# Performance work log

Measured on AMD Instinct MI355X. Metric: run time of the kernel, lower is better.

The kernel has to match this reference:

```python
import jax, jax.numpy as jnp
import numpy as np
from jax import lax

B, NQ, C = 2, 1024, 2048
H, DH = 16, 128
G, CD = 4, 512          # off_grps, off_dim = C // G
LR, HR = 24, 72         # low-res grid side, high-res grid side
INTER = 64
K = LR * LR             # sampled K/V tokens (grid_size == lr_size)


def setup_inputs() -> dict:
    key = jax.random.key(0)
    ks = jax.random.split(key, 16)
    s = 0.02
    d = {}
    d['hidden_states'] = jax.random.normal(ks[0], (B, NQ, C), jnp.float32)
    d['image_hd'] = jax.random.normal(ks[1], (B, HR * HR, C), jnp.float32)
    d['wq'] = jax.random.normal(ks[2], (C, C), jnp.float32) * s
    d['wk'] = jax.random.normal(ks[3], (C, C), jnp.float32) * s
    d['wv'] = jax.random.normal(ks[4], (C, C), jnp.float32) * s
    d['wo'] = jax.random.normal(ks[5], (C, C), jnp.float32) * s
    d['conv_dw_w'] = jax.random.normal(ks[6], (CD, 1, 3, 3), jnp.float32) * s
    d['ln1_w'] = jnp.ones((CD,), jnp.float32)
    d['ln1_b'] = jnp.zeros((CD,), jnp.float32)
    d['conv_lr_proj_w'] = jax.random.normal(ks[7], (INTER, CD), jnp.float32) * s
    d['proj_int_w'] = jax.random.normal(ks[8], (INTER, CD), jnp.float32) * s
    d['proj_int_b'] = jnp.zeros((INTER,), jnp.float32)
    d['ln2_w'] = jnp.ones((INTER,), jnp.float32)
    d['ln2_b'] = jnp.zeros((INTER,), jnp.float32)
    d['conv_off_w'] = jax.random.normal(ks[9], (2, INTER), jnp.float32) * s
    d['k_hd_w'] = jax.random.normal(ks[10], (C, C), jnp.float32) * s
    d['k_hd_b'] = jnp.zeros((C,), jnp.float32)
    d['v_hd_w'] = jax.random.normal(ks[11], (C, C), jnp.float32) * s
    d['v_hd_b'] = jnp.zeros((C,), jnp.float32)
    return d


def _ln_channels(x, w, b, eps=1e-5):
    # LayerNorm2d: normalize over channel axis of [N, C, H, W]
    mu = jnp.mean(x, axis=1, keepdims=True)
    var = jnp.var(x, axis=1, keepdims=True)
    xn = (x - mu) * lax.rsqrt(var + eps)
    return xn * w[None, :, None, None] + b[None, :, None, None]


def _tokens_to_grid(x, S):
    # [B, S*S, C] -> [B*G, CD, S, S]  (group channels like einops '(b) (h w) (g c) -> (b g) c h w')
    return x.reshape(B, S, S, G, CD).transpose(0, 3, 4, 1, 2).reshape(B * G, CD, S, S)


def _bilinear_sample(img, grid):
    # img [N, C, Hh, Wh]; grid [N, K, 2] (x, y) normalized to [-1, 1], align_corners=True
    N, Cc, Hh, Wh = img.shape
    x = (grid[..., 0] + 1.0) * 0.5 * (Wh - 1)
    y = (grid[..., 1] + 1.0) * 0.5 * (Hh - 1)
    x0f, y0f = jnp.floor(x), jnp.floor(y)
    wx = (x - x0f)[:, None, :]
    wy = (y - y0f)[:, None, :]
    x0 = jnp.clip(x0f.astype(jnp.int32), 0, Wh - 1)
    x1 = jnp.clip(x0 + 1, 0, Wh - 1)
    y0 = jnp.clip(y0f.astype(jnp.int32), 0, Hh - 1)
    y1 = jnp.clip(y0 + 1, 0, Hh - 1)
    imgf = img.reshape(N, Cc, Hh * Wh)
    gather = jax.vmap(lambda im, ix: im[:, ix])  # ([C,HW],[K]) -> [C,K]
    v00 = gather(imgf, y0 * Wh + x0)
    v01 = gather(imgf, y0 * Wh + x1)
    v10 = gather(imgf, y1 * Wh + x0)
    v11 = gather(imgf, y1 * Wh + x1)
    return (v00 * (1 - wx) * (1 - wy) + v01 * wx * (1 - wy)
            + v10 * (1 - wx) * wy + v11 * wx * wy)  # [N, C, K]


def _ref_grid():
    # normalized reference points as in _grid_generate (centers / (S-1) * 2 - 1)
    yy = (jnp.linspace(0.5, LR - 0.5, LR) / (LR - 1.0)) * 2.0 - 1.0
    xx = (jnp.linspace(0.5, LR - 0.5, LR) / (LR - 1.0)) * 2.0 - 1.0
    gy, gx = jnp.meshgrid(yy, xx, indexing='ij')
    return jnp.stack([gx, gy], axis=-1).reshape(K, 2)  # (x, y)


def reference(hidden_states, image_hd, wq, wk, wv, wo, conv_dw_w, ln1_w, ln1_b,
              conv_lr_proj_w, proj_int_w, proj_int_b, ln2_w, ln2_b, conv_off_w,
              k_hd_w, k_hd_b, v_hd_w, v_hd_b):
    # ---- QKV on the full sequence ----
    q = hidden_states @ wq.T
    k_txt = hidden_states @ wk.T
    v_txt = hidden_states @ wv.T

    # ---- offset network on LR image tokens (first LR*LR tokens) ----
    lr = _tokens_to_grid(hidden_states[:, :K, :], LR)          # [B*G, CD, LR, LR]
    x = lax.conv_general_dilated(lr, conv_dw_w, (1, 1), 'SAME',
                                 feature_group_count=CD,
                                 dimension_numbers=('NCHW', 'OIHW', 'NCHW'))
    x = jax.nn.silu(x)
    x = _ln_channels(x, ln1_w, ln1_b)
    x = jnp.einsum('nchw,oc->nohw', x, conv_lr_proj_w)          # 1x1 conv -> [B*G, INTER, LR, LR]
    # intention gate from spatially pooled group features
    pooled = jnp.mean(lr, axis=(2, 3))                          # [B*G, CD]
    gate = jax.nn.sigmoid(pooled @ proj_int_w.T + proj_int_b)   # [B*G, INTER]
    x = x * gate[:, :, None, None]
    x = _ln_channels(x, ln2_w, ln2_b)
    off = jnp.einsum('nchw,oc->nohw', x, conv_off_w)            # [B*G, 2, LR, LR]
    off = off.transpose(0, 2, 3, 1).reshape(B * G, K, 2)        # (x, y)
    pos = jnp.tanh(_ref_grid()[None] + off)                     # sampling locs in [-1, 1]

    # ---- deformable gather from HD features ----
    hd = _tokens_to_grid(image_hd, HR)                          # [B*G, CD, HR, HR]
    samp = _bilinear_sample(hd, pos)                            # [B*G, CD, K]
    samp = samp.reshape(B, G, CD, K).transpose(0, 3, 1, 2).reshape(B, K, C)
    k_hd = samp @ k_hd_w.T + k_hd_b
    v_hd = samp @ v_hd_w.T + v_hd_b

    # ---- attention: causal over text tokens, HD tokens fully visible ----
    k_all = jnp.concatenate([k_txt, k_hd], axis=1)              # [B, NQ+K, C]
    v_all = jnp.concatenate([v_txt, v_hd], axis=1)
    qh = q.reshape(B, NQ, H, DH).transpose(0, 2, 1, 3)
    kh = k_all.reshape(B, NQ + K, H, DH).transpose(0, 2, 1, 3)
    vh = v_all.reshape(B, NQ + K, H, DH).transpose(0, 2, 1, 3)
    scores = jnp.einsum('bhqd,bhkd->bhqk', qh, kh) / jnp.sqrt(jnp.float32(DH))
    col = jnp.arange(NQ + K)
    row = jnp.arange(NQ)
    allow = (col[None, :] >= NQ) | (col[None, :] <= row[:, None])
    scores = jnp.where(allow[None, None], scores, jnp.float32(-1e9))
    attn = jax.nn.softmax(scores, axis=-1)
    out = jnp.einsum('bhqk,bhkd->bhqd', attn, vh)
    out = out.transpose(0, 2, 1, 3).reshape(B, NQ, C)
    return out @ wo.T
```

## Files before the change

### kernel.cpp

```cpp
#include <hip/hip_runtime.h>

typedef unsigned short u16;
typedef unsigned int u32;
typedef __attribute__((ext_vector_type(8))) short bf8;
typedef __attribute__((ext_vector_type(4))) float f4;
typedef __attribute__((ext_vector_type(4))) unsigned short us4;

constexpr int B = 2;
constexpr int NQ = 1024;
constexpr int C = 2048;
constexpr int DH = 128;
constexpr int G = 4;
constexpr int CD = 512;
constexpr int LR = 24;
constexpr int HR = 72;
constexpr int INTER = 64;
constexpr int K = LR * LR;
constexpr int NKV = NQ + K;

#define MFMA16(a, b, c) __builtin_amdgcn_mfma_f32_16x16x32_bf16(a, b, c, 0, 0, 0)
#define GLDS(g, l)                                                         \
  __builtin_amdgcn_global_load_lds(                                        \
      (const __attribute__((address_space(1))) void*)(g),                  \
      (__attribute__((address_space(3))) void*)(l), 16, 0, 0)

__device__ __forceinline__ u16 f2bf1(float f) {
  u32 u = __float_as_uint(f);
  u32 r = (u + 0x7fffu + ((u >> 16) & 1u)) >> 16;
  return (u16)r;
}

__global__ __launch_bounds__(256) void f2bf_k8(
    const float* __restrict__ s0, const float* __restrict__ s1,
    const float* __restrict__ s2, const float* __restrict__ s3,
    const float* __restrict__ s4, const float* __restrict__ s5,
    const float* __restrict__ s6, const float* __restrict__ plrw,
    u16* __restrict__ d0, u16* __restrict__ d1, u16* __restrict__ d2,
    u16* __restrict__ d3, u16* __restrict__ d4, u16* __restrict__ d5,
    u16* __restrict__ d6, float* __restrict__ wt) {
  __shared__ u16 L[64][68];
  const int y = blockIdx.y;
  const int t = threadIdx.x;
  if (y == 7) {
    if (blockIdx.x >= 128) return;
    const int idx = blockIdx.x * 256 + t;
    wt[idx] = plrw[(idx & 63) * 512 + (idx >> 6)];
    return;
  }
  const float* s;
  u16* d;
  switch (y) {
    case 0: s = s0; d = d0; break;
    case 1: s = s1; d = d1; break;
    case 2: s = s2; d = d2; break;
    case 3: s = s3; d = d3; break;
    case 4: s = s4; d = d4; break;
    case 5: s = s5; d = d5; break;
    default: s = s6; d = d6; break;
  }
  if (y < 5) {
    const int pc = blockIdx.x;
    const int mb = pc >> 5, kb = pc & 31;
    const int rin = t >> 2, c0 = (t & 3) * 16;
    const float* src = s + (size_t)(mb * 64 + rin) * 2048 + kb * 64 + c0;
#pragma unroll
    for (int j = 0; j < 16; j += 4) {
      float4 v = *(const float4*)(src + j);
      L[rin][c0 + j] = f2bf1(v.x);
      L[rin][c0 + j + 1] = f2bf1(v.y);
      L[rin][c0 + j + 2] = f2bf1(v.z);
      L[rin][c0 + j + 3] = f2bf1(v.w);
    }
    __syncthreads();
    u16* dst = d + (size_t)pc * 4096 + t * 16;
#pragma unroll
    for (int gg = 0; gg < 2; ++gg) {
      const int g = t * 2 + gg;
      const int rh = g & 15, ks2 = (g >> 4) & 3, kc = (g >> 6) & 1, fr = g >> 7;
      const int row = fr * 16 + rh, cc = kc * 32 + ks2 * 8;
      us4 o0, o1;
      o0.x = L[row][cc];     o0.y = L[row][cc + 1];
      o0.z = L[row][cc + 2]; o0.w = L[row][cc + 3];
      o1.x = L[row][cc + 4]; o1.y = L[row][cc + 5];
      o1.z = L[row][cc + 6]; o1.w = L[row][cc + 7];
      *(us4*)(dst + gg * 8) = o0;
      *(us4*)(dst + gg * 8 + 4) = o1;
    }
  } else {
    const size_t i0 = ((size_t)blockIdx.x * 256 + t) * 16;
#pragma unroll
    for (int j = 0; j < 16; j += 4) {
      float4 v = *(const float4*)(s + i0 + j);
      us4 o;
      o.x = f2bf1(v.x); o.y = f2bf1(v.y); o.z = f2bf1(v.z); o.w = f2bf1(v.w);
      *(us4*)(d + i0 + j) = o;
    }
  }
}

#define SB()                               \
  do {                                     \
    __builtin_amdgcn_sched_barrier(0);     \
    __builtin_amdgcn_s_barrier();          \
    __builtin_amdgcn_sched_barrier(0);     \
  } while (0)
#define WVM(n) asm volatile("s_waitcnt vmcnt(" #n ")" ::: "memory")

__global__ __launch_bounds__(512, 2) void gemm_fused(
    const u16* __restrict__ Ast, const u16* __restrict__ Wq,
    const u16* __restrict__ Wk, const u16* __restrict__ Wv,
    const u16* __restrict__ samp, const u16* __restrict__ khw,
    const u16* __restrict__ vhw, const float* __restrict__ khb,
    const float* __restrict__ vhb, u16* __restrict__ outq,
    u16* __restrict__ kg, u16* __restrict__ vg) {
  __shared__ u16 As[2][4][4096];
  __shared__ u16 Bs[2][4][4096];
  const int tid = threadIdx.x, lane = tid & 63, w = tid >> 6;
  const int ks = lane >> 4, r = lane & 15;
  const int bid = blockIdx.x;

  if (bid < 192) {
    const int wm = w >> 2, wn = w & 3;
    const int swz = (bid & 7) * 24 + (bid >> 3);
    const int mt = swz / 24, nt = swz % 24;
    const u16* Wst = (nt < 8) ? Wq : (nt < 16) ? Wk : Wv;
    const int nb0 = (nt & 7) * 4;
    const int mb0 = mt * 4;

#define ST_A03(bi, kt)                                                        \
  do {                                                                        \
    GLDS(Ast + ((size_t)(mb0 + 0) * 32 + (kt)) * 4096 + tid * 8,              \
         &As[bi][0][tid * 8]);                                                \
    GLDS(Ast + ((size_t)(mb0 + 2) * 32 + (kt)) * 4096 + tid * 8,              \
         &As[bi][2][tid * 8]);                                                \
  } while (0)
#define ST_A47(bi, kt)                                                        \
  do {                                                                        \
    GLDS(Ast + ((size_t)(mb0 + 1) * 32 + (kt)) * 4096 + tid * 8,              \
         &As[bi][1][tid * 8]);                                                \
    GLDS(Ast + ((size_t)(mb0 + 3) * 32 + (kt)) * 4096 + tid * 8,              \
         &As[bi][3][tid * 8]);                                                \
  } while (0)
#define ST_B01(bi, kt)                                                        \
  do {                                                                        \
    GLDS(Wst + ((size_t)(nb0 + 0) * 32 + (kt)) * 4096 + tid * 8,              \
         &Bs[bi][0][tid * 8]);                                                \
    GLDS(Wst + ((size_t)(nb0 + 1) * 32 + (kt)) * 4096 + tid * 8,              \
         &Bs[bi][1][tid * 8]);                                                \
  } while (0)
#define ST_B23(bi, kt)                                                        \
  do {                                                                        \
    GLDS(Wst + ((size_t)(nb0 + 2) * 32 + (kt)) * 4096 + tid * 8,              \
         &Bs[bi][2][tid * 8]);                                                \
    GLDS(Wst + ((size_t)(nb0 + 3) * 32 + (kt)) * 4096 + tid * 8,              \
         &Bs[bi][3][tid * 8]);                                                \
  } while (0)
#define RD_A(dst, bi, half, kc)                                               \
  _Pragma("unroll") for (int i2 = 0; i2 < 4; ++i2) dst[i2] =                  \
      *(const bf8*)(&As[bi][wm * 2 + (half)]                                  \
                       [((i2 * 2 + (kc)) * 4 + ks) * 128 + r * 8]);
#define RD_B(dst, bi, kc)                                                     \
  _Pragma("unroll") for (int j2 = 0; j2 < 4; ++j2) dst[j2] =                  \
      *(const bf8*)(&Bs[bi][wn][((j2 * 2 + (kc)) * 4 + ks) * 128 + r * 8]);
#define MM(ACC, AF, BF)                                                       \
  do {                                                                        \
    __builtin_amdgcn_s_setprio(1);                                            \
    _Pragma("unroll") for (int i3 = 0; i3 < 4; ++i3)                          \
        _Pragma("unroll") for (int j3 = 0; j3 < 4; ++j3) ACC[i3][j3] =        \
            MFMA16(AF[i3], BF[j3], ACC[i3][j3]);                              \
    __builtin_amdgcn_s_setprio(0);                                            \
  } while (0)

    f4 accA[4][4], accB[4][4];
#pragma unroll
    for (int i = 0; i < 4; ++i)
#pragma unroll
      for (int j = 0; j < 4; ++j) {
        accA[i][j] = f4{0.f, 0.f, 0.f, 0.f};
        accB[i][j] = f4{0.f, 0.f, 0.f, 0.f};
      }
    bf8 af[4], b0[4], b1[4];

    ST_A03(0, 0); ST_B01(0, 0); ST_B23(0, 0); ST_A47(0, 0);
    ST_A03(1, 1); ST_B01(1, 1);
    WVM(6);
    SB();

    for (int t = 0; t < 32; ++t) {
      const int buf = t & 1;
      RD_A(af, buf, 0, 0);
      RD_B(b0, buf, 0);
      if (t + 1 < 32) ST_B23(buf ^ 1, t + 1);
      SB();
      MM(accA, af, b0);
      SB();
      RD_A(af, buf, 0, 1);
      RD_B(b1, buf, 1);
      if (t + 1 < 32) ST_A47(buf ^ 1, t + 1);
      SB();
      MM(accA, af, b1);
      if (t + 1 < 32) { WVM(8); } else { WVM(0); }
      SB();
      RD_A(af, buf, 1, 0);
      if (t + 2 < 32) ST_A03(buf, t + 2);
      SB();
      MM(accB, af, b0);
      SB();
      RD_A(af, buf, 1, 1);
      if (t + 2 < 32) ST_B01(buf, t + 2);
      SB();
      MM(accB, af, b1);
      if (t + 2 < 32) { WVM(6); } else if (t + 1 < 32) { WVM(2); }
      SB();
    }

#define EPI(ACC, HALF)                                                        \
  _Pragma("unroll") for (int i = 0; i < 4; ++i)                               \
      _Pragma("unroll") for (int j = 0; j < 4; ++j)                           \
          _Pragma("unroll") for (int rr = 0; rr < 4; ++rr) {                  \
    const int m = mt * 256 + wm * 128 + (HALF)*64 + i * 16 + ks * 4 + rr;     \
    const int n = nt * 256 + wn * 64 + j * 16 + r;                            \
    const float v = ACC[i][j][rr];                                            \
    const int sel = n >> 11, nn = n & 2047, hh = nn >> 7, dd = nn & 127;      \
    const int bb = m >> 10, qq = m & 1023;                                    \
    const u16 bv = f2bf1(v);                                                  \
    if (sel == 0) {                                                           \
      outq[(size_t)m * 2048 + nn] = bv;                                       \
    } else if (sel == 1) {                                                    \
      kg[(((size_t)(bb * 16 + hh) * 50 + (qq >> 5)) * 16 + (dd >> 3)) * 256 + \
         (qq & 31) * 8 + (dd & 7)] = bv;                                      \
    } else {                                                                  \
      vg[((size_t)(bb * 16 + hh) * 200 + (qq >> 3)) * 1024 + dd * 8 +         \
         (qq & 7)] = bv;                                                      \
    }                                                                         \
  }
    EPI(accA, 0)
    EPI(accB, 1)
#undef EPI
  } else {
    const int hb = bid - 192;
    const int mt = hb >> 4, nb = hb & 15;
    const int m0 = mt * 128, n0l = nb * 128;
    const int srow = lane >> 2, scol = (lane & 3) * 8;
    const int wh = w & 3;
    const int wr = wh >> 1, wc = wh & 1;
    const bool is_v = (w >= 4);
    const u16* Wp = is_v ? vhw : khw;
    const float* bias = is_v ? vhb : khb;

#define HDST(bi, k0)                                                          \
  do {                                                                        \
    GLDS(samp + (size_t)(m0 + w * 16 + srow) * 2048 + scol + (k0),            \
         &As[bi][0][w * 512 + lane * 8]);                                     \
    GLDS(Wp + (size_t)(n0l + wh * 32 + srow) * 2048 + scol + (k0),            \
         &Bs[bi][is_v ? 1 : 0][wh * 1024 + lane * 8]);                        \
    GLDS(Wp + (size_t)(n0l + wh * 32 + 16 + srow) * 2048 + scol + (k0),       \
         &Bs[bi][is_v ? 1 : 0][wh * 1024 + 512 + lane * 8]);                  \
  } while (0)

    f4 acc[4][4];
#pragma unroll
    for (int i = 0; i < 4; ++i)
#pragma unroll
      for (int j = 0; j < 4; ++j) acc[i][j] = f4{0.f, 0.f, 0.f, 0.f};
    const int koff = ks * 8;
    const int arow = wr * 64 + r, brow = wc * 64 + r;

    HDST(0, 0);
    int cur = 0;
    for (int k0 = 0; k0 < 2048; k0 += 32) {
      __syncthreads();
      if (k0 + 32 < 2048) HDST(cur ^ 1, k0 + 32);
      bf8 af2[4], bw[4];
#pragma unroll
      for (int i = 0; i < 4; ++i)
        af2[i] = *(const bf8*)(&As[cur][0][(arow + i * 16) * 32 + koff]);
#pragma unroll
      for (int j = 0; j < 4; ++j)
        bw[j] =
            *(const bf8*)(&Bs[cur][is_v ? 1 : 0][(brow + j * 16) * 32 + koff]);
#pragma unroll
      for (int i = 0; i < 4; ++i)
#pragma unroll
        for (int j = 0; j < 4; ++j)
          acc[i][j] = MFMA16(af2[i], bw[j], acc[i][j]);
      cur ^= 1;
    }
#undef HDST
    const int rbase = ks * 4;
#pragma unroll
    for (int i = 0; i < 4; ++i) {
#pragma unroll
      for (int j = 0; j < 4; ++j) {
        const int nn = n0l + wc * 64 + j * 16 + r;
        const int hh = nn >> 7, dd = nn & 127;
#pragma unroll
        for (int rr = 0; rr < 4; ++rr) {
          const int m = m0 + wr * 64 + i * 16 + rbase + rr;
          const int bb = m / 576;
          const int kv = 1024 + (m - bb * 576);
          const u16 bv = f2bf1(acc[i][j][rr] + bias[nn]);
          if (!is_v) {
            kg[(((size_t)(bb * 16 + hh) * 50 + (kv >> 5)) * 16 + (dd >> 3)) *
                   256 +
               (kv & 31) * 8 + (dd & 7)] = bv;
          } else {
            vg[((size_t)(bb * 16 + hh) * 200 + (kv >> 3)) * 1024 + dd * 8 +
               (kv & 7)] = bv;
          }
        }
      }
    }
  }
}

__global__ __launch_bounds__(256) void gemm_out_st(const u16* __restrict__ Ast2,
                                                   const u16* __restrict__ Wst,
                                                   float* __restrict__ outf) {
  __shared__ u16 As2[2][2][4096];
  __shared__ u16 Ws2[2][2][4096];
  const int tid = threadIdx.x, lane = tid & 63, w = tid >> 6;
  const int wr = w >> 1, wc = w & 1;
  const int ks = lane >> 4, r = lane & 15;
  const int mt = blockIdx.y, nt = blockIdx.x;

#define OST(bi, kt)                                                           \
  do {                                                                        \
    const size_t a0 = ((size_t)(mt * 2 + 0) * 32 + (kt)) * 4096;              \
    const size_t a1 = ((size_t)(mt * 2 + 1) * 32 + (kt)) * 4096;              \
    const size_t w0 = ((size_t)(nt * 2 + 0) * 32 + (kt)) * 4096;              \
    const size_t w1 = ((size_t)(nt * 2 + 1) * 32 + (kt)) * 4096;              \
    GLDS(Ast2 + a0 + tid * 8, &As2[bi][0][tid * 8]);                          \
    GLDS(Ast2 + a0 + 2048 + tid * 8, &As2[bi][0][2048 + tid * 8]);            \
    GLDS(Ast2 + a1 + tid * 8, &As2[bi][1][tid * 8]);                          \
    GLDS(Ast2 + a1 + 2048 + tid * 8, &As2[bi][1][2048 + tid * 8]);            \
    GLDS(Wst + w0 + tid * 8, &Ws2[bi][0][tid * 8]);                           \
    GLDS(Wst + w0 + 2048 + tid * 8, &Ws2[bi][0][2048 + tid * 8]);             \
    GLDS(Wst + w1 + tid * 8, &Ws2[bi][1][tid * 8]);                           \
    GLDS(Wst + w1 + 2048 + tid * 8, &Ws2[bi][1][2048 + tid * 8]);             \
  } while (0)

  f4 acc[4][4];
#pragma unroll
  for (int i = 0; i < 4; ++i)
#pragma unroll
    for (int j = 0; j < 4; ++j) acc[i][j] = f4{0.f, 0.f, 0.f, 0.f};

  OST(0, 0);
  int cur = 0;
  for (int kt = 0; kt < 32; ++kt) {
    __syncthreads();
    if (kt + 1 < 32) OST(cur ^ 1, kt + 1);
#pragma unroll
    for (int kc = 0; kc < 2; ++kc) {
      bf8 a_[4], b_[4];
#pragma unroll
      for (int i = 0; i < 4; ++i)
        a_[i] = *(const bf8*)(&As2[cur][wr][((i * 2 + kc) * 4 + ks) * 128 +
                                            r * 8]);
#pragma unroll
      for (int j = 0; j < 4; ++j)
        b_[j] = *(const bf8*)(&Ws2[cur][wc][((j * 2 + kc) * 4 + ks) * 128 +
                                            r * 8]);
#pragma unroll
      for (int i = 0; i < 4; ++i)
#pragma unroll
        for (int j = 0; j < 4; ++j)
          acc[i][j] = MFMA16(a_[i], b_[j], acc[i][j]);
    }
    cur ^= 1;
  }
#undef OST
#pragma unroll
  for (int i = 0; i < 4; ++i)
#pragma unroll
    for (int j = 0; j < 4; ++j) {
      const int n = nt * 128 + wc * 64 + j * 16 + r;
#pragma unroll
      for (int rr = 0; rr < 4; ++rr) {
        const int m = mt * 128 + wr * 64 + i * 16 + ks * 4 + rr;
        outf[(size_t)m * 2048 + n] = acc[i][j][rr];
      }
    }
}

__global__ __launch_bounds__(256) void dwpool(const float* __restrict__ hs,
                                              const float* __restrict__ cw,
                                              float* __restrict__ x1,
                                              float* __restrict__ pooled) {
  __shared__ float L[32][577];
  const int bidx = blockIdx.x;
  const int n = bidx >> 4, cg = bidx & 15;
  const int b = n >> 2, g = n & 3;
  const int c0 = cg * 32;
  const int t = threadIdx.x;
  {
    const int c = t & 31, pr = t >> 5;
    const float* src = hs + (size_t)b * 1024 * 2048 + g * 512 + c0 + c;
#pragma unroll 4
    for (int j = 0; j < 72; ++j) {
      const int p = j * 8 + pr;
      L[c][p] = src[(size_t)p * 2048];
    }
  }
  __syncthreads();
  {
    const int c = t >> 3, seg = t & 7;
    float s = 0.f;
    for (int i = 0; i < 72; ++i) s += L[c][seg * 72 + i];
    s += __shfl_xor(s, 1);
    s += __shfl_xor(s, 2);
    s += __shfl_xor(s, 4);
    if (seg == 0) pooled[n * 512 + c0 + c] = s * (1.f / 576.f);
  }
  const size_t base_out = (size_t)(n * 512 + c0) * 576;
  for (int j = 0; j < 72; ++j) {
    const int idx = j * 256 + t;
    const int c = idx / 576, p = idx - c * 576;
    const int y = p / 24, x = p - y * 24;
    const float* wp = cw + (c0 + c) * 9;
    float s = 0.f;
#pragma unroll
    for (int dy = -1; dy <= 1; ++dy)
#pragma unroll
      for (int dx = -1; dx <= 1; ++dx) {
        const int yy = y + dy, xx = x + dx;
        if (yy < 0 || yy >= 24 || xx < 0 || xx >= 24) continue;
        s += L[c][yy * 24 + xx] * wp[(dy + 1) * 3 + dx + 1];
      }
    x1[base_out + idx] = s / (1.f + expf(-s));
  }
}

__global__ __launch_bounds__(256) void lnproj(const float* __restrict__ x1,
                                              const float* __restrict__ ln1w,
                                              const float* __restrict__ ln1b,
                                              const float* __restrict__ wt,
                                              float* __restrict__ x2) {
  __shared__ float Xs[512][68];
  __shared__ float rs[4][64], rss[4][64];
  const int bidx = blockIdx.x;
  const int n = bidx / 9, pc = bidx % 9;
  const int p0 = pc * 64;
  const int t = threadIdx.x;
  {
    const int pl = t & 63, c4 = t >> 6;
    const float* src = x1 + (size_t)n * 512 * 576 + p0 + pl;
#pragma unroll 4
    for (int j = 0; j < 128; ++j) {
      const int c = j * 4 + c4;
      Xs[c][pl] = src[(size_t)c * 576];
    }
  }
  __syncthreads();
  {
    const int pl = t & 63, q = t >> 6;
    float s = 0.f, ss = 0.f;
    for (int c = q * 128; c < q * 128 + 128; ++c) {
      const float v = Xs[c][pl];
      s += v;
      ss += v * v;
    }
    rs[q][pl] = s;
    rss[q][pl] = ss;
    __syncthreads();
    const float S = rs[0][pl] + rs[1][pl] + rs[2][pl] + rs[3][pl];
    const float SS = rss[0][pl] + rss[1][pl] + rss[2][pl] + rss[3][pl];
    const float mean = S * (1.f / 512.f);
    const float inv = rsqrtf(SS * (1.f / 512.f) - mean * mean + 1e-5f);
    for (int c = q * 128; c < q * 128 + 128; ++c)
      Xs[c][pl] = (Xs[c][pl] - mean) * inv * ln1w[c] + ln1b[c];
  }
  __syncthreads();
  {
    const int o4 = (t & 15) * 4, pl0 = (t >> 4) * 4;
    float acc[4][4] = {};
    for (int c = 0; c < 512; ++c) {
      const f4 xv = *(const f4*)(&Xs[c][pl0]);
      const f4 wv = *(const f4*)(&wt[c * 64 + o4]);
#pragma unroll
      for (int i = 0; i < 4; ++i)
#pragma unroll
        for (int j = 0; j < 4; ++j) acc[i][j] += wv[i] * xv[j];
    }
#pragma unroll
    for (int i = 0; i < 4; ++i) {
      f4 ov;
      ov[0] = acc[i][0]; ov[1] = acc[i][1];
      ov[2] = acc[i][2]; ov[3] = acc[i][3];
      *(f4*)(&x2[(size_t)(n * 64 + o4 + i) * 576 + p0 + pl0]) = ov;
    }
  }
}

__global__ __launch_bounds__(64) void gate_k(const float* __restrict__ pooled,
                                             const float* __restrict__ w,
                                             const float* __restrict__ bias,
                                             float* __restrict__ gate) {
  int idx = blockIdx.x * 64 + threadIdx.x;
  if (idx >= B * G * INTER) return;
  int n = idx >> 6, o = idx & 63;
  const float* pb = pooled + n * CD;
  const float* wb = w + o * CD;
  float s = bias[o];
  for (int c = 0; c < CD; ++c) s += pb[c] * wb[c];
  gate[idx] = 1.f / (1.f + expf(-s));
}

__global__ __launch_bounds__(256) void ln2_off_pos(
    const float* __restrict__ x2, const float* __restrict__ gate,
    const float* __restrict__ ln2w, const float* __restrict__ ln2b,
    const float* __restrict__ offw, float* __restrict__ pos) {
  int wid = (blockIdx.x * 256 + threadIdx.x) >> 6;
  int lane = threadIdx.x & 63;
  if (wid >= B * G * K) return;
  int n = wid / K, p = wid % K;
  float v = x2[((size_t)n * INTER + lane) * K + p] * gate[n * INTER + lane];
  float s = v, ss = v * v;
  for (int o = 32; o; o >>= 1) {
    s += __shfl_xor(s, o);
    ss += __shfl_xor(ss, o);
  }
  float mean = s * (1.f / INTER);
  float var = ss * (1.f / INTER) - mean * mean;
  float xn = (v - mean) * rsqrtf(var + 1e-5f) * ln2w[lane] + ln2b[lane];
  float ox = xn * offw[lane];
  float oy = xn * offw[INTER + lane];
  for (int o = 32; o; o >>= 1) {
    ox += __shfl_xor(ox, o);
    oy += __shfl_xor(oy, o);
  }
  if (lane == 0) {
    int yi = p / LR, xi = p % LR;
    float rx = (xi + 0.5f) / 23.f * 2.f - 1.f;
    float ry = (yi + 0.5f) / 23.f * 2.f - 1.f;
    pos[((size_t)n * K + p) * 2 + 0] = tanhf(rx + ox);
    pos[((size_t)n * K + p) * 2 + 1] = tanhf(ry + oy);
  }
}

__global__ __launch_bounds__(256) void sample_k(const float* __restrict__ img,
                                                const float* __restrict__ pos,
                                                u16* __restrict__ samp) {
  const int bk = blockIdx.x;
  const int b = bk / K, k = bk % K;
  __shared__ int s_idx[G][4];
  __shared__ float s_w[G][4];
  if (threadIdx.x < G) {
    int g = threadIdx.x;
    int n = b * G + g;
    float px = pos[((size_t)n * K + k) * 2 + 0];
    float py = pos[((size_t)n * K + k) * 2 + 1];
    float x = (px + 1.f) * 0.5f * (HR - 1);
    float y = (py + 1.f) * 0.5f * (HR - 1);
    float x0f = floorf(x), y0f = floorf(y);
    float wx = x - x0f, wy = y - y0f;
    int x0 = min(max((int)x0f, 0), HR - 1);
    int x1 = min(x0 + 1, HR - 1);
    int y0 = min(max((int)y0f, 0), HR - 1);
    int y1 = min(y0 + 1, HR - 1);
    s_idx[g][0] = y0 * HR + x0;
    s_idx[g][1] = y0 * HR + x1;
    s_idx[g][2] = y1 * HR + x0;
    s_idx[g][3] = y1 * HR + x1;
    s_w[g][0] = (1.f - wx) * (1.f - wy);
    s_w[g][1] = wx * (1.f - wy);
    s_w[g][2] = (1.f - wx) * wy;
    s_w[g][3] = wx * wy;
  }
  __syncthreads();
  const float* ib = img + (size_t)b * HR * HR * C;
  u16* ob = samp + ((size_t)b * K + k) * C;
  for (int ch = threadIdx.x; ch < C; ch += 256) {
    int g = ch >> 9;
    float v = s_w[g][0] * ib[(size_t)s_idx[g][0] * C + ch] +
              s_w[g][1] * ib[(size_t)s_idx[g][1] * C + ch] +
              s_w[g][2] * ib[(size_t)s_idx[g][2] * C + ch] +
              s_w[g][3] * ib[(size_t)s_idx[g][3] * C + ch];
    ob[ch] = f2bf1(v);
  }
}

__global__ __launch_bounds__(256) void attn_part(
    const u16* __restrict__ qb, const u16* __restrict__ kg,
    const u16* __restrict__ vg, float* __restrict__ oA,
    float* __restrict__ oB, float* __restrict__ mlA,
    float* __restrict__ mlB) {
  const int i = blockIdx.x;
  const int fam = i >> 9;
  const int r9 = i & 511;
  int bh, qblk;
  if (fam == 0) {
    const int pair = r9 & 255, half = r9 >> 8;
    bh = pair & 31;
    const int q8 = pair >> 5;
    qblk = half ? (15 - q8) : q8;
  } else {
    bh = r9 & 31;
    qblk = r9 >> 5;
  }
  const int b = bh >> 4, h = bh & 15;
  const int q0 = qblk * 64;
  const int tid = threadIdx.x, lane = tid & 63, w = tid >> 6;
  const int qw = q0 + w * 16;
  const int col = lane & 15, kpart = lane >> 4, rbase = kpart * 4;
  __shared__ u16 Ks[2][4096];
  __shared__ u16 Vs[2][4096];
  __shared__ u16 Pl[4][16 * 40];
  float* oacc = fam ? oB : oA;
  float* ml = fam ? mlB : mlA;
  bf8 qf[4];
  {
    const u16* qp =
        qb + (size_t)(b * 1024 + qw + col) * 2048 + h * 128 + kpart * 8;
#pragma unroll
    for (int dc = 0; dc < 4; ++dc) qf[dc] = *(const bf8*)(qp + dc * 32);
  }
  f4 o[8];
#pragma unroll
  for (int df = 0; df < 8; ++df) o[df] = f4{0.f, 0.f, 0.f, 0.f};
  float m_r[4] = {-1e30f, -1e30f, -1e30f, -1e30f};
  float l_p[4] = {0.f, 0.f, 0.f, 0.f};
  const float scale = 0.08838834764831845f;
  const int nt = fam ? 18 : ((q0 + 64) >> 5);
  const int kvadd = fam ? 1024 : 0;
  const u16* kbh = kg + (size_t)bh * (NKV * 128);
  const u16* vbh = vg + (size_t)bh * (NKV * 128);
  u16* pw = &Pl[w][0];

#define ASTAGE(bi, kv0)                                                       \
  do {                                                                        \
    const u16* gk = kbh + (size_t)((kv0) >> 5) * 4096 + w * 1024 + lane * 8;  \
    GLDS(gk, &Ks[bi][w * 1024 + lane * 8]);                                   \
    GLDS(gk + 512, &Ks[bi][w * 1024 + 512 + lane * 8]);                       \
    const u16* gv = vbh + (size_t)((kv0) >> 3) * 1024 + w * 1024 + lane * 8;  \
    GLDS(gv, &Vs[bi][w * 1024 + lane * 8]);                                   \
    GLDS(gv + 512, &Vs[bi][w * 1024 + 512 + lane * 8]);                       \
  } while (0)

  ASTAGE(0, kvadd);
  int cur = 0;
  for (int t = 0; t < nt; ++t) {
    const int kv0 = kvadd + (t << 5);
    __syncthreads();
    if (t + 1 < nt) ASTAGE(cur ^ 1, kvadd + ((t + 1) << 5));
    const u16* ksb = &Ks[cur][0];
    const u16* vsb = &Vs[cur][0];
    f4 s0 = {0.f, 0.f, 0.f, 0.f}, s1 = {0.f, 0.f, 0.f, 0.f};
    __builtin_amdgcn_s_setprio(1);
#pragma unroll
    for (int dc = 0; dc < 4; ++dc) {
      const int dblk = dc * 4 + kpart;
      bf8 k0f = *(const bf8*)(ksb + (dblk * 32 + col) * 8);
      bf8 k1f = *(const bf8*)(ksb + (dblk * 32 + 16 + col) * 8);
      s0 = MFMA16(qf[dc], k0f, s0);
      s1 = MFMA16(qf[dc], k1f, s1);
    }
    __builtin_amdgcn_s_setprio(0);
    float sa[4], sc[4], loc[4], p0[4], p1[4];
    bool grow = false;
    const bool need_mask = (fam == 0) && (kv0 + 31 > qw);
#pragma unroll
    for (int rr = 0; rr < 4; ++rr) {
      float a = s0[rr] * scale, c2 = s1[rr] * scale;
      if (need_mask) {
        const int qg = qw + rbase + rr;
        if (kv0 + col > qg) a = -1e30f;
        if (kv0 + 16 + col > qg) c2 = -1e30f;
      }
      sa[rr] = a; sc[rr] = c2;
      loc[rr] = fmaxf(a, c2);
      grow |= (loc[rr] > m_r[rr] + 8.f);
    }
    if (__any(grow)) {
      float fr[4];
#pragma unroll
      for (int rr = 0; rr < 4; ++rr) {
        float mx = loc[rr];
        mx = fmaxf(mx, __shfl_xor(mx, 1));
        mx = fmaxf(mx, __shfl_xor(mx, 2));
        mx = fmaxf(mx, __shfl_xor(mx, 4));
        mx = fmaxf(mx, __shfl_xor(mx, 8));
        const float mn = fmaxf(m_r[rr], mx);
        fr[rr] = __expf(m_r[rr] - mn);
        m_r[rr] = mn;
        p0[rr] = __expf(sa[rr] - mn);
        p1[rr] = __expf(sc[rr] - mn);
        l_p[rr] = l_p[rr] * fr[rr] + p0[rr] + p1[rr];
      }
#pragma unroll
      for (int df = 0; df < 8; ++df) {
        o[df][0] *= fr[0]; o[df][1] *= fr[1];
        o[df][2] *= fr[2]; o[df][3] *= fr[3];
      }
    } else {
#pragma unroll
      for (int rr = 0; rr < 4; ++rr) {
        p0[rr] = __expf(sa[rr] - m_r[rr]);
        p1[rr] = __expf(sc[rr] - m_r[rr]);
        l_p[rr] += p0[rr] + p1[rr];
      }
    }
#pragma unroll
    for (int rr = 0; rr < 4; ++rr) {
      pw[(rbase + rr) * 40 + col] = f2bf1(p0[rr]);
      pw[(rbase + rr) * 40 + 16 + col] = f2bf1(p1[rr]);
    }
    bf8 pa = *(const bf8*)(pw + col * 40 + kpart * 8);
    __builtin_amdgcn_s_setprio(1);
#pragma unroll
    for (int df = 0; df < 8; ++df) {
      bf8 vf = *(const bf8*)(vsb + (kpart * 128 + df * 16 + col) * 8);
      o[df] = MFMA16(pa, vf, o[df]);
    }
    __builtin_amdgcn_s_setprio(0);
    cur ^= 1;
  }
#undef ASTAGE
  float l_r[4];
#pragma unroll
  for (int rr = 0; rr < 4; ++rr) {
    float ps = l_p[rr];
    ps += __shfl_xor(ps, 1);
    ps += __shfl_xor(ps, 2);
    ps += __shfl_xor(ps, 4);
    ps += __shfl_xor(ps, 8);
    l_r[rr] = ps;
  }
  float* orow = oacc + (size_t)(bh * 1024 + qw + rbase) * 128 + col;
#pragma unroll
  for (int df = 0; df < 8; ++df)
#pragma unroll
    for (int rr = 0; rr < 4; ++rr)
      orow[(size_t)rr * 128 + df * 16] = o[df][rr];
  if (col == 0) {
#pragma unroll
    for (int rr = 0; rr < 4; ++rr) {
      const int row = bh * 1024 + qw + rbase + rr;
      ml[row * 2] = m_r[rr];
      ml[row * 2 + 1] = l_r[rr];
    }
  }
}

__global__ __launch_bounds__(256) void attn_merge(
    const float* __restrict__ oA, const float* __restrict__ mlA,
    const float* __restrict__ oB, const float* __restrict__ mlB,
    u16* __restrict__ aob_st) {
  const int gid = blockIdx.x * 256 + threadIdx.x;
  const int row = gid >> 5;
  const int d0 = (gid & 31) * 4;
  const float mA = mlA[row * 2], lA = mlA[row * 2 + 1];
  const float mB = mlB[row * 2], lB = mlB[row * 2 + 1];
  const float m = fmaxf(mA, mB);
  const float wA = __expf(mA - m), wB = __expf(mB - m);
  const float inv = 1.f / (lA * wA + lB * wB);
  const f4 a = *(const f4*)(oA + (size_t)row * 128 + d0);
  const f4 c = *(const f4*)(oB + (size_t)row * 128 + d0);
  const int bh = row >> 10, q = row & 1023;
  const int bb = bh >> 4, h = bh & 15;
  const int mm = bb * 1024 + q;
  const int col = h * 128 + d0;
  const int mb = mm >> 6, fr = (mm >> 4) & 3, r = mm & 15;
  const int kb = col >> 6, kc = (col >> 5) & 1, ks = (col >> 3) & 3,
            j0 = col & 7;
  u16* dst = aob_st + ((size_t)(mb * 32 + kb)) * 4096 +
             (((fr * 2 + kc) * 4 + ks) * 16 + r) * 8 + j0;
  us4 ov;
  ov.x = f2bf1((a[0] * wA + c[0] * wB) * inv);
  ov.y = f2bf1((a[1] * wA + c[1] * wB) * inv);
  ov.z = f2bf1((a[2] * wA + c[2] * wB) * inv);
  ov.w = f2bf1((a[3] * wA + c[3] * wB) * inv);
  *(us4*)dst = ov;
}

extern "C" void kernel_launch(void* const* d_in, const int* in_sizes, int n_in,
                              void* d_out, int out_size, void* d_ws,
                              size_t ws_size, hipStream_t stream) {
  const float* hs = (const float*)d_in[0];
  const float* img = (const float*)d_in[1];
  const float* wq = (const float*)d_in[2];
  const float* wk = (const float*)d_in[3];
  const float* wv = (const float*)d_in[4];
  const float* wo = (const float*)d_in[5];
  const float* cdw = (const float*)d_in[6];
  const float* ln1w = (const float*)d_in[7];
  const float* ln1b = (const float*)d_in[8];
  const float* plrw = (const float*)d_in[9];
  const float* piw = (const float*)d_in[10];
  const float* pib = (const float*)d_in[11];
  const float* ln2w = (const float*)d_in[12];
  const float* ln2b = (const float*)d_in[13];
  const float* offw = (const float*)d_in[14];
  const float* khw = (const float*)d_in[15];
  const float* khb = (const float*)d_in[16];
  const float* vhw = (const float*)d_in[17];
  const float* vhb = (const float*)d_in[18];
  float* outp = (float*)d_out;

  u16* wsp = (u16*)d_ws;
  const size_t SZ = 4194304;
  u16* hs_st = wsp;
  u16* wq_st = wsp + SZ;
  u16* wk_st = wsp + 2 * SZ;
  u16* wv_st = wsp + 3 * SZ;
  u16* wo_st = wsp + 4 * SZ;
  u16* khw_bf = wsp + 5 * SZ;
  u16* vhw_bf = wsp + 6 * SZ;
  u16* qb_bf = wsp + 7 * SZ;
  u16* samp_bf = wsp + 8 * SZ;
  u16* kg = wsp + 8 * SZ + 2359296;
  u16* vg = kg + 6553600;
  float* x1b = (float*)kg + 2359296;
  float* x2b = x1b + 2359296;
  float* poolb = x2b + 294912;
  float* gb = poolb + 4096;
  float* posb = (float*)(vg + 6553600);
  float* mlA = posb + 9216;
  float* mlB = mlA + 65536;
  float* wtb = mlB + 65536;
  float* oA = (float*)(wsp + 2 * SZ);
  float* oB = (float*)(wsp + 5 * SZ);
  u16* aob_st = wq_st;

  dim3 blk(256);
  dwpool<<<dim3(128), blk, 0, stream>>>(hs, cdw, x1b, poolb);
  f2bf_k8<<<dim3(1024, 8), blk, 0, stream>>>(hs, wq, wk, wv, wo, khw, vhw,
                                             plrw, hs_st, wq_st, wk_st, wv_st,
                                             wo_st, khw_bf, vhw_bf, wtb);
  lnproj<<<dim3(72), blk, 0, stream>>>(x1b, ln1w, ln1b, wtb, x2b);
  gate_k<<<dim3(8), dim3(64), 0, stream>>>(poolb, piw, pib, gb);
  ln2_off_pos<<<dim3(1152), blk, 0, stream>>>(x2b, gb, ln2w, ln2b, offw, posb);
  sample_k<<<dim3(B * K), blk, 0, stream>>>(img, posb, samp_bf);

  gemm_fused<<<dim3(336), dim3(512), 0, stream>>>(
      hs_st, wq_st, wk_st, wv_st, samp_bf, khw_bf, vhw_bf, khb, vhb, qb_bf,
      kg, vg);
  attn_part<<<dim3(1024), blk, 0, stream>>>(qb_bf, kg, vg, oA, oB, mlA, mlB);
  attn_merge<<<dim3(4096), blk, 0, stream>>>(oA, mlA, oB, mlB, aob_st);
  gemm_out_st<<<dim3(16, 16), blk, 0, stream>>>(aob_st, wo_st, outp);
}
```

Measured before the change: 367.8 us.

## Fuse preprocessing kernels and add explicit vmcnt waits with MFMA priority

Merges the depthwise-conv/pool kernel into the bf16 conversion launch as an extra grid row, folds the gate computation into the LN-projection kernel, and fuses offset/position computation into the bilinear sampling kernel, cutting the launch count from ten to seven. The GEMM and attention loops replace __syncthreads with split barriers plus explicit s_waitcnt vmcnt counts so the next tile's async loads stay in flight, and they raise wave priority around the MFMA blocks. The conversion kernel's shared buffer grows to about 74 KB for every block, which may reduce occupancy for the conversion blocks. The vmcnt values must match the number of outstanding loads issued per stage.

Result: faster. 346.1 us (-5.9%).

```diff
diff --git a/kernel.cpp b/kernel.cpp
--- a/kernel.cpp
+++ b/kernel.cpp
@@ -23,6 +23,17 @@
   __builtin_amdgcn_global_load_lds(                                        \
       (const __attribute__((address_space(1))) void*)(g),                  \
       (__attribute__((address_space(3))) void*)(l), 16, 0, 0)
+#define SB()                               \
+  do {                                     \
+    __builtin_amdgcn_sched_barrier(0);     \
+    __builtin_amdgcn_s_barrier();          \
+    __builtin_amdgcn_sched_barrier(0);     \
+  } while (0)
+#define WVM(n)                                              \
+  do {                                                      \
+    asm volatile("s_waitcnt vmcnt(" #n ")" ::: "memory");   \
+    __builtin_amdgcn_sched_barrier(0);                      \
+  } while (0)
 
 __device__ __forceinline__ u16 f2bf1(float f) {
   u32 u = __float_as_uint(f);
@@ -30,21 +41,65 @@
   return (u16)r;
 }
 
-__global__ __launch_bounds__(256) void f2bf_k8(
+__global__ __launch_bounds__(256) void f2bf_k9(
     const float* __restrict__ s0, const float* __restrict__ s1,
     const float* __restrict__ s2, const float* __restrict__ s3,
     const float* __restrict__ s4, const float* __restrict__ s5,
     const float* __restrict__ s6, const float* __restrict__ plrw,
-    u16* __restrict__ d0, u16* __restrict__ d1, u16* __restrict__ d2,
-    u16* __restrict__ d3, u16* __restrict__ d4, u16* __restrict__ d5,
-    u16* __restrict__ d6, float* __restrict__ wt) {
-  __shared__ u16 L[64][68];
+    const float* __restrict__ cdw, u16* __restrict__ d0, u16* __restrict__ d1,
+    u16* __restrict__ d2, u16* __restrict__ d3, u16* __restrict__ d4,
+    u16* __restrict__ d5, u16* __restrict__ d6, float* __restrict__ wt,
+    float* __restrict__ x1, float* __restrict__ pooled) {
+  __shared__ float SH[32 * 577];
   const int y = blockIdx.y;
   const int t = threadIdx.x;
   if (y == 7) {
     if (blockIdx.x >= 128) return;
     const int idx = blockIdx.x * 256 + t;
     wt[idx] = plrw[(idx & 63) * 512 + (idx >> 6)];
+    return;
+  }
+  if (y == 8) {
+    if (blockIdx.x >= 128) return;
+    const int n = blockIdx.x >> 4, cg = blockIdx.x & 15;
+    const int b = n >> 2, g = n & 3;
+    const int c0 = cg * 32;
+    {
+      const int c = t & 31, pr = t >> 5;
+      const float* src = s0 + (size_t)b * 1024 * 2048 + g * 512 + c0 + c;
+#pragma unroll 4
+      for (int j = 0; j < 72; ++j) {
+        const int p = j * 8 + pr;
+        SH[c * 577 + p] = src[(size_t)p * 2048];
+      }
+    }
+    __syncthreads();
+    {
+      const int c = t >> 3, seg = t & 7;
+      float s = 0.f;
+      for (int i = 0; i < 72; ++i) s += SH[c * 577 + seg * 72 + i];
+      s += __shfl_xor(s, 1);
+      s += __shfl_xor(s, 2);
+      s += __shfl_xor(s, 4);
+      if (seg == 0) pooled[n * 512 + c0 + c] = s * (1.f / 576.f);
+    }
+    const size_t base_out = (size_t)(n * 512 + c0) * 576;
+    for (int j = 0; j < 72; ++j) {
+      const int idx = j * 256 + t;
+      const int c = idx / 576, p = idx - c * 576;
+      const int yy0 = p / 24, xx0 = p - yy0 * 24;
+      const float* wp = cdw + (c0 + c) * 9;
+      float s = 0.f;
+#pragma unroll
+      for (int dy = -1; dy <= 1; ++dy)
+#pragma unroll
+        for (int dx = -1; dx <= 1; ++dx) {
+          const int yy = yy0 + dy, xx = xx0 + dx;
+          if (yy < 0 || yy >= 24 || xx < 0 || xx >= 24) continue;
+          s += SH[c * 577 + yy * 24 + xx] * wp[(dy + 1) * 3 + dx + 1];
+        }
+      x1[base_out + idx] = s / (1.f + expf(-s));
+    }
     return;
   }
   const float* s;
@@ -59,6 +114,7 @@
     default: s = s6; d = d6; break;
   }
   if (y < 5) {
+    u16* L = (u16*)SH;
     const int pc = blockIdx.x;
     const int mb = pc >> 5, kb = pc & 31;
     const int rin = t >> 2, c0 = (t & 3) * 16;
@@ -66,10 +122,10 @@
 #pragma unroll
     for (int j = 0; j < 16; j += 4) {
       float4 v = *(const float4*)(src + j);
-      L[rin][c0 + j] = f2bf1(v.x);
-      L[rin][c0 + j + 1] = f2bf1(v.y);
-      L[rin][c0 + j + 2] = f2bf1(v.z);
-      L[rin][c0 + j + 3] = f2bf1(v.w);
+      L[rin * 68 + c0 + j] = f2bf1(v.x);
+      L[rin * 68 + c0 + j + 1] = f2bf1(v.y);
+      L[rin * 68 + c0 + j + 2] = f2bf1(v.z);
+      L[rin * 68 + c0 + j + 3] = f2bf1(v.w);
     }
     __syncthreads();
     u16* dst = d + (size_t)pc * 4096 + t * 16;
@@ -79,10 +135,10 @@
       const int rh = g & 15, ks2 = (g >> 4) & 3, kc = (g >> 6) & 1, fr = g >> 7;
       const int row = fr * 16 + rh, cc = kc * 32 + ks2 * 8;
       us4 o0, o1;
-      o0.x = L[row][cc];     o0.y = L[row][cc + 1];
-      o0.z = L[row][cc + 2]; o0.w = L[row][cc + 3];
-      o1.x = L[row][cc + 4]; o1.y = L[row][cc + 5];
-      o1.z = L[row][cc + 6]; o1.w = L[row][cc + 7];
+      o0.x = L[row * 68 + cc];     o0.y = L[row * 68 + cc + 1];
+      o0.z = L[row * 68 + cc + 2]; o0.w = L[row * 68 + cc + 3];
+      o1.x = L[row * 68 + cc + 4]; o1.y = L[row * 68 + cc + 5];
+      o1.z = L[row * 68 + cc + 6]; o1.w = L[row * 68 + cc + 7];
       *(us4*)(dst + gg * 8) = o0;
       *(us4*)(dst + gg * 8 + 4) = o1;
     }
@@ -97,14 +153,6 @@
     }
   }
 }
-
-#define SB()                               \
-  do {                                     \
-    __builtin_amdgcn_sched_barrier(0);     \
-    __builtin_amdgcn_s_barrier();          \
-    __builtin_amdgcn_sched_barrier(0);     \
-  } while (0)
-#define WVM(n) asm volatile("s_waitcnt vmcnt(" #n ")" ::: "memory")
 
 __global__ __launch_bounds__(512, 2) void gemm_fused(
     const u16* __restrict__ Ast, const u16* __restrict__ Wq,
@@ -269,8 +317,14 @@
     HDST(0, 0);
     int cur = 0;
     for (int k0 = 0; k0 < 2048; k0 += 32) {
-      __syncthreads();
-      if (k0 + 32 < 2048) HDST(cur ^ 1, k0 + 32);
+      SB();
+      if (k0 + 32 < 2048) {
+        HDST(cur ^ 1, k0 + 32);
+        WVM(3);
+      } else {
+        WVM(0);
+      }
+      SB();
       bf8 af2[4], bw[4];
 #pragma unroll
       for (int i = 0; i < 4; ++i)
@@ -279,11 +333,13 @@
       for (int j = 0; j < 4; ++j)
         bw[j] =
             *(const bf8*)(&Bs[cur][is_v ? 1 : 0][(brow + j * 16) * 32 + koff]);
+      __builtin_amdgcn_s_setprio(1);
 #pragma unroll
       for (int i = 0; i < 4; ++i)
 #pragma unroll
         for (int j = 0; j < 4; ++j)
           acc[i][j] = MFMA16(af2[i], bw[j], acc[i][j]);
+      __builtin_amdgcn_s_setprio(0);
       cur ^= 1;
     }
 #undef HDST
@@ -349,8 +405,14 @@
   OST(0, 0);
   int cur = 0;
   for (int kt = 0; kt < 32; ++kt) {
-    __syncthreads();
-    if (kt + 1 < 32) OST(cur ^ 1, kt + 1);
+    SB();
+    if (kt + 1 < 32) {
+      OST(cur ^ 1, kt + 1);
+      WVM(8);
+    } else {
+      WVM(0);
+    }
+    SB();
 #pragma unroll
     for (int kc = 0; kc < 2; ++kc) {
       bf8 a_[4], b_[4];
@@ -362,11 +424,13 @@
       for (int j = 0; j < 4; ++j)
         b_[j] = *(const bf8*)(&Ws2[cur][wc][((j * 2 + kc) * 4 + ks) * 128 +
                                             r * 8]);
+      __builtin_amdgcn_s_setprio(1);
 #pragma unroll
       for (int i = 0; i < 4; ++i)
 #pragma unroll
         for (int j = 0; j < 4; ++j)
           acc[i][j] = MFMA16(a_[i], b_[j], acc[i][j]);
+      __builtin_amdgcn_s_setprio(0);
     }
     cur ^= 1;
   }
@@ -384,65 +448,28 @@
     }
 }
 
-__global__ __launch_bounds__(256) void dwpool(const float* __restrict__ hs,
-                                              const float* __restrict__ cw,
-                                              float* __restrict__ x1,
-                                              float* __restrict__ pooled) {
-  __shared__ float L[32][577];
-  const int bidx = blockIdx.x;
-  const int n = bidx >> 4, cg = bidx & 15;
-  const int b = n >> 2, g = n & 3;
-  const int c0 = cg * 32;
-  const int t = threadIdx.x;
-  {
-    const int c = t & 31, pr = t >> 5;
-    const float* src = hs + (size_t)b * 1024 * 2048 + g * 512 + c0 + c;
-#pragma unroll 4
-    for (int j = 0; j < 72; ++j) {
-      const int p = j * 8 + pr;
-      L[c][p] = src[(size_t)p * 2048];
-    }
-  }
-  __syncthreads();
-  {
-    const int c = t >> 3, seg = t & 7;
-    float s = 0.f;
-    for (int i = 0; i < 72; ++i) s += L[c][seg * 72 + i];
-    s += __shfl_xor(s, 1);
-    s += __shfl_xor(s, 2);
-    s += __shfl_xor(s, 4);
-    if (seg == 0) pooled[n * 512 + c0 + c] = s * (1.f / 576.f);
-  }
-  const size_t base_out = (size_t)(n * 512 + c0) * 576;
-  for (int j = 0; j < 72; ++j) {
-    const int idx = j * 256 + t;
-    const int c = idx / 576, p = idx - c * 576;
-    const int y = p / 24, x = p - y * 24;
-    const float* wp = cw + (c0 + c) * 9;
-    float s = 0.f;
-#pragma unroll
-    for (int dy = -1; dy <= 1; ++dy)
-#pragma unroll
-      for (int dx = -1; dx <= 1; ++dx) {
-        const int yy = y + dy, xx = x + dx;
-        if (yy < 0 || yy >= 24 || xx < 0 || xx >= 24) continue;
-        s += L[c][yy * 24 + xx] * wp[(dy + 1) * 3 + dx + 1];
-      }
-    x1[base_out + idx] = s / (1.f + expf(-s));
-  }
-}
-
-__global__ __launch_bounds__(256) void lnproj(const float* __restrict__ x1,
-                                              const float* __restrict__ ln1w,
-                                              const float* __restrict__ ln1b,
-                                              const float* __restrict__ wt,
-                                              float* __restrict__ x2) {
+__global__ __launch_bounds__(256) void lnproj_gate(
+    const float* __restrict__ x1, const float* __restrict__ ln1w,
+    const float* __restrict__ ln1b, const float* __restrict__ wt,
+    const float* __restrict__ pooled, const float* __restrict__ piw,
+    const float* __restrict__ pib, float* __restrict__ x2,
+    float* __restrict__ gate) {
   __shared__ float Xs[512][68];
   __shared__ float rs[4][64], rss[4][64];
   const int bidx = blockIdx.x;
+  const int t = threadIdx.x;
+  if (bidx >= 72) {
+    const int idx = (bidx - 72) * 256 + t;
+    const int n = idx >> 6, o = idx & 63;
+    const float* pb = pooled + n * 512;
+    const float* wb = piw + o * 512;
+    float s = pib[o];
+    for (int c = 0; c < 512; ++c) s += pb[c] * wb[c];
+    gate[idx] = 1.f / (1.f + expf(-s));
+    return;
+  }
   const int n = bidx / 9, pc = bidx % 9;
   const int p0 = pc * 64;
-  const int t = threadIdx.x;
   {
     const int pl = t & 63, c4 = t >> 6;
     const float* src = x1 + (size_t)n * 512 * 576 + p0 + pl;
@@ -493,90 +520,66 @@
   }
 }
 
-__global__ __launch_bounds__(64) void gate_k(const float* __restrict__ pooled,
-                                             const float* __restrict__ w,
-                                             const float* __restrict__ bias,
-                                             float* __restrict__ gate) {
-  int idx = blockIdx.x * 64 + threadIdx.x;
-  if (idx >= B * G * INTER) return;
-  int n = idx >> 6, o = idx & 63;
-  const float* pb = pooled + n * CD;
-  const float* wb = w + o * CD;
-  float s = bias[o];
-  for (int c = 0; c < CD; ++c) s += pb[c] * wb[c];
-  gate[idx] = 1.f / (1.f + expf(-s));
-}
-
-__global__ __launch_bounds__(256) void ln2_off_pos(
+__global__ __launch_bounds__(256) void pos_sample(
     const float* __restrict__ x2, const float* __restrict__ gate,
     const float* __restrict__ ln2w, const float* __restrict__ ln2b,
-    const float* __restrict__ offw, float* __restrict__ pos) {
-  int wid = (blockIdx.x * 256 + threadIdx.x) >> 6;
-  int lane = threadIdx.x & 63;
-  if (wid >= B * G * K) return;
-  int n = wid / K, p = wid % K;
-  float v = x2[((size_t)n * INTER + lane) * K + p] * gate[n * INTER + lane];
-  float s = v, ss = v * v;
-  for (int o = 32; o; o >>= 1) {
-    s += __shfl_xor(s, o);
-    ss += __shfl_xor(ss, o);
-  }
-  float mean = s * (1.f / INTER);
-  float var = ss * (1.f / INTER) - mean * mean;
-  float xn = (v - mean) * rsqrtf(var + 1e-5f) * ln2w[lane] + ln2b[lane];
-  float ox = xn * offw[lane];
-  float oy = xn * offw[INTER + lane];
-  for (int o = 32; o; o >>= 1) {
-    ox += __shfl_xor(ox, o);
-    oy += __shfl_xor(oy, o);
-  }
-  if (lane == 0) {
-    int yi = p / LR, xi = p % LR;
-    float rx = (xi + 0.5f) / 23.f * 2.f - 1.f;
-    float ry = (yi + 0.5f) / 23.f * 2.f - 1.f;
-    pos[((size_t)n * K + p) * 2 + 0] = tanhf(rx + ox);
-    pos[((size_t)n * K + p) * 2 + 1] = tanhf(ry + oy);
-  }
-}
-
-__global__ __launch_bounds__(256) void sample_k(const float* __restrict__ img,
-                                                const float* __restrict__ pos,
-                                                u16* __restrict__ samp) {
+    const float* __restrict__ offw, const float* __restrict__ img,
+    u16* __restrict__ samp) {
   const int bk = blockIdx.x;
   const int b = bk / K, k = bk % K;
   __shared__ int s_idx[G][4];
   __shared__ float s_w[G][4];
-  if (threadIdx.x < G) {
-    int g = threadIdx.x;
-    int n = b * G + g;
-    float px = pos[((size_t)n * K + k) * 2 + 0];
-    float py = pos[((size_t)n * K + k) * 2 + 1];
-    float x = (px + 1.f) * 0.5f * (HR - 1);
-    float y = (py + 1.f) * 0.5f * (HR - 1);
-    float x0f = floorf(x), y0f = floorf(y);
-    float wx = x - x0f, wy = y - y0f;
-    int x0 = min(max((int)x0f, 0), HR - 1);
-    int x1 = min(x0 + 1, HR - 1);
-    int y0 = min(max((int)y0f, 0), HR - 1);
-    int y1 = min(y0 + 1, HR - 1);
-    s_idx[g][0] = y0 * HR + x0;
-    s_idx[g][1] = y0 * HR + x1;
-    s_idx[g][2] = y1 * HR + x0;
-    s_idx[g][3] = y1 * HR + x1;
-    s_w[g][0] = (1.f - wx) * (1.f - wy);
-    s_w[g][1] = wx * (1.f - wy);
-    s_w[g][2] = (1.f - wx) * wy;
-    s_w[g][3] = wx * wy;
+  const int t = threadIdx.x;
+  const int g = t >> 6, lane = t & 63;
+  {
+    const int n = b * G + g;
+    float v = x2[((size_t)n * INTER + lane) * K + k] * gate[n * INTER + lane];
+    float s = v, ss = v * v;
+    for (int o = 32; o; o >>= 1) {
+      s += __shfl_xor(s, o);
+      ss += __shfl_xor(ss, o);
+    }
+    const float mean = s * (1.f / INTER);
+    const float var = ss * (1.f / INTER) - mean * mean;
+    const float xn = (v - mean) * rsqrtf(var + 1e-5f) * ln2w[lane] + ln2b[lane];
+    float ox = xn * offw[lane];
+    float oy = xn * offw[INTER + lane];
+    for (int o = 32; o; o >>= 1) {
+      ox += __shfl_xor(ox, o);
+      oy += __shfl_xor(oy, o);
+    }
+    if (lane == 0) {
+      const int yi = k / LR, xi = k % LR;
+      const float rx = (xi + 0.5f) / 23.f * 2.f - 1.f;
+      const float ry = (yi + 0.5f) / 23.f * 2.f - 1.f;
+      const float px = tanhf(rx + ox), py = tanhf(ry + oy);
+      const float x = (px + 1.f) * 0.5f * (HR - 1);
+      const float y = (py + 1.f) * 0.5f * (HR - 1);
+      const float x0f = floorf(x), y0f = floorf(y);
+      const float wx = x - x0f, wy = y - y0f;
+      const int x0 = min(max((int)x0f, 0), HR - 1);
+      const int x1 = min(x0 + 1, HR - 1);
+      const int y0 = min(max((int)y0f, 0), HR - 1);
+      const int y1 = min(y0 + 1, HR - 1);
+      s_idx[g][0] = y0 * HR + x0;
+      s_idx[g][1] = y0 * HR + x1;
+      s_idx[g][2] = y1 * HR + x0;
+      s_idx[g][3] = y1 * HR + x1;
+      s_w[g][0] = (1.f - wx) * (1.f - wy);
+      s_w[g][1] = wx * (1.f - wy);
+      s_w[g][2] = (1.f - wx) * wy;
+      s_w[g][3] = wx * wy;
+    }
   }
   __syncthreads();
   const float* ib = img + (size_t)b * HR * HR * C;
   u16* ob = samp + ((size_t)b * K + k) * C;
-  for (int ch = threadIdx.x; ch < C; ch += 256) {
-    int g = ch >> 9;
-    float v = s_w[g][0] * ib[(size_t)s_idx[g][0] * C + ch] +
-              s_w[g][1] * ib[(size_t)s_idx[g][1] * C + ch] +
-              s_w[g][2] * ib[(size_t)s_idx[g][2] * C + ch] +
-              s_w[g][3] * ib[(size_t)s_idx[g][3] * C + ch];
+  for (int ch = t; ch < C; ch += 256) {
+    const int gg = ch >> 9;
+    float v = s_w[gg][0] * ib[(size_t)s_idx[gg][0] * C + ch] +
+              s_w[gg][1] * ib[(size_t)s_idx[gg][1] * C + ch] +
+              s_w[gg][2] * ib[(size_t)s_idx[gg][2] * C + ch] +
+              s_w[gg][3] * ib[(size_t)s_idx[gg][3] * C + ch];
     ob[ch] = f2bf1(v);
   }
 }
@@ -642,8 +645,14 @@
   int cur = 0;
   for (int t = 0; t < nt; ++t) {
     const int kv0 = kvadd + (t << 5);
-    __syncthreads();
-    if (t + 1 < nt) ASTAGE(cur ^ 1, kvadd + ((t + 1) << 5));
+    SB();
+    if (t + 1 < nt) {
+      ASTAGE(cur ^ 1, kvadd + ((t + 1) << 5));
+      WVM(4);
+    } else {
+      WVM(0);
+    }
+    SB();
     const u16* ksb = &Ks[cur][0];
     const u16* vsb = &Vs[cur][0];
     f4 s0 = {0.f, 0.f, 0.f, 0.f}, s1 = {0.f, 0.f, 0.f, 0.f};
@@ -824,15 +833,13 @@
   u16* aob_st = wq_st;
 
   dim3 blk(256);
-  dwpool<<<dim3(128), blk, 0, stream>>>(hs, cdw, x1b, poolb);
-  f2bf_k8<<<dim3(1024, 8), blk, 0, stream>>>(hs, wq, wk, wv, wo, khw, vhw,
-                                             plrw, hs_st, wq_st, wk_st, wv_st,
-                                             wo_st, khw_bf, vhw_bf, wtb);
-  lnproj<<<dim3(72), blk, 0, stream>>>(x1b, ln1w, ln1b, wtb, x2b);
-  gate_k<<<dim3(8), dim3(64), 0, stream>>>(poolb, piw, pib, gb);
-  ln2_off_pos<<<dim3(1152), blk, 0, stream>>>(x2b, gb, ln2w, ln2b, offw, posb);
-  sample_k<<<dim3(B * K), blk, 0, stream>>>(img, posb, samp_bf);
-
+  f2bf_k9<<<dim3(1024, 9), blk, 0, stream>>>(
+      hs, wq, wk, wv, wo, khw, vhw, plrw, cdw, hs_st, wq_st, wk_st, wv_st,
+      wo_st, khw_bf, vhw_bf, wtb, x1b, poolb);
+  lnproj_gate<<<dim3(74), blk, 0, stream>>>(x1b, ln1w, ln1b, wtb, poolb, piw,
+                                            pib, x2b, gb);
+  pos_sample<<<dim3(B * K), blk, 0, stream>>>(x2b, gb, ln2w, ln2b, offw, img,
+                                              samp_bf);
   gemm_fused<<<dim3(336), dim3(512), 0, stream>>>(
       hs_st, wq_st, wk_st, wv_st, samp_bf, khw_bf, vhw_bf, khb, vhb, qb_bf,
       kg, vg);
```
